# Optimization experiments

Hardware: AMD Instinct MI355X
Metric: run time of the kernel (lower is better)

The kernel has to match this reference:

```python
import jax, jax.numpy as jnp
import numpy as np

N = 100000   # nodes
E = 1600000  # edges
F_IN = 256   # input features
H = 128      # hidden
C = 40       # classes


def setup_inputs() -> dict:
    key = jax.random.key(0)
    ks = jax.random.split(key, 6)
    x = jax.random.normal(ks[0], (N, F_IN), dtype=jnp.float32)
    edge_index = jax.random.randint(ks[1], (2, E), 0, N, dtype=jnp.int32)
    edge_attr = jax.random.uniform(ks[2], (E,), dtype=jnp.float32)
    # Glorot-style init like GCNConv
    W1 = jax.random.normal(ks[3], (F_IN, H), dtype=jnp.float32) * (1.0 / np.sqrt(F_IN))
    b1 = jnp.zeros((H,), dtype=jnp.float32)
    W2 = jax.random.normal(ks[4], (H, C), dtype=jnp.float32) * (1.0 / np.sqrt(H))
    b2 = jnp.zeros((C,), dtype=jnp.float32)
    return {"x": x, "edge_index": edge_index, "edge_attr": edge_attr,
            "W1": W1, "b1": b1, "W2": W2, "b2": b2}


def _gcn_norm(edge_index, edge_weight, num_nodes):
    # PyG gcn_norm: add self-loops (weight 1), symmetric D^{-1/2} A D^{-1/2}
    row, col = edge_index[0], edge_index[1]
    loop = jnp.arange(num_nodes, dtype=row.dtype)
    row = jnp.concatenate([row, loop])
    col = jnp.concatenate([col, loop])
    ew = jnp.concatenate([edge_weight, jnp.ones((num_nodes,), edge_weight.dtype)])
    deg = jax.ops.segment_sum(ew, col, num_segments=num_nodes)
    dinv = jnp.where(deg > 0, jax.lax.rsqrt(deg), 0.0)
    norm = dinv[row] * ew * dinv[col]
    return row, col, norm


def _gcn_conv(x, row, col, norm, W, b):
    h = x @ W                              # [N, out] dense transform first
    msg = h[row] * norm[:, None]           # gather source + edge scaling
    out = jax.ops.segment_sum(msg, col, num_segments=x.shape[0])  # scatter-add
    return out + b


def reference(x, edge_index, edge_attr, W1, b1, W2, b2):
    row, col, norm = _gcn_norm(edge_index, edge_attr, x.shape[0])
    h = _gcn_conv(x, row, col, norm, W1, b1)
    h = jax.nn.relu(h)
    # dropout is identity in eval mode
    h = _gcn_conv(h, row, col, norm, W2, b2)
    return jax.nn.log_softmax(h, axis=1)
```

## Files before the change

### kernel.cpp

```cpp
#include <hip/hip_runtime.h>

#define N_NODES 100000
#define N_EDGES 1600000
#define F_INPUT 256
#define H_DIM   128
#define C_DIM   40
#define NBKT    391
#define NCHK    1563
#define NGEMM1  1563

typedef short  bf8   __attribute__((ext_vector_type(8)));
typedef float  f32x4 __attribute__((ext_vector_type(4)));
typedef float  f32x2 __attribute__((ext_vector_type(2)));
typedef unsigned short u16x8 __attribute__((ext_vector_type(8)));

static __device__ __forceinline__ unsigned short f2bf(float f) {
    union { float f; unsigned u; } v; v.f = f;
    unsigned r = v.u + 0x7FFFu + ((v.u >> 16) & 1u);
    return (unsigned short)(r >> 16);
}
static __device__ __forceinline__ f32x2 bfpair(unsigned u) {
    union { unsigned u; float f; } lo, hi;
    lo.u = u << 16; hi.u = u & 0xFFFF0000u;
    return (f32x2){lo.f, hi.f};
}

__global__ void k_pre(const float* __restrict__ W1, const float* __restrict__ W2,
                      unsigned short* Wp1, unsigned short* Wp2) {
    int idx = blockIdx.x * 256 + threadIdx.x;
    if (idx < 32768) {
        int j = idx & 7, lane = (idx >> 3) & 63, ks = (idx >> 9) & 7, nt = idx >> 12;
        int m = lane & 15, q = lane >> 4;
        Wp1[idx] = f2bf(W1[(ks * 32 + q * 8 + j) * H_DIM + nt * 16 + m]);
    }
    int idx2 = idx - 32768;
    if (idx2 >= 0 && idx2 < 6144) {
        int j = idx2 & 7, lane = (idx2 >> 3) & 63, ks = (idx2 >> 9) & 3, nt = idx2 >> 11;
        int m = lane & 15, q = lane >> 4;
        int n = nt * 16 + m;
        Wp2[idx2] = (n < C_DIM) ? f2bf(W2[(ks * 32 + q * 8 + j) * C_DIM + n]) : (unsigned short)0;
    }
}

__global__ void k_hist(const int* __restrict__ col, unsigned* __restrict__ histG) {
    __shared__ unsigned histL[NBKT];
    int chunk = blockIdx.x, tid = threadIdx.x;
    for (int i = tid; i < NBKT; i += 256) histL[i] = 0;
    __syncthreads();
    int e0 = chunk * 1024 + tid;
#pragma unroll
    for (int k = 0; k < 4; k++) {
        int e = e0 + k * 256;
        if (e < N_EDGES) atomicAdd(&histL[col[e] >> 8], 1u);
    }
    __syncthreads();
    for (int i = tid; i < NBKT; i += 256) histG[(size_t)i * NCHK + chunk] = histL[i];
}

__global__ __launch_bounds__(256, 2) void k_gemm1(
        const float* __restrict__ x, const unsigned short* __restrict__ Wp,
        unsigned short* __restrict__ h) {
    __shared__ unsigned short sWp[32768];
    __shared__ unsigned short lds_out[64 * H_DIM];
    int tid = threadIdx.x;
    int wave = tid >> 6, lane = tid & 63;
    int m = lane & 15, q = lane >> 4;
    int tile = blockIdx.x;
    int row0 = tile * 64 + wave * 16;
    int rowA = row0 + m; if (rowA >= N_NODES) rowA = N_NODES - 1;
    const float* xr = x + (long)rowA * F_INPUT + q * 8;

    float4 xv[16];
#pragma unroll
    for (int ks = 0; ks < 8; ks++) {
        xv[2 * ks]     = *(const float4*)(xr + ks * 32);
        xv[2 * ks + 1] = *(const float4*)(xr + ks * 32 + 4);
    }
#pragma unroll
    for (int it = 0; it < 16; it++) {
        int idx = (it * 256 + tid) * 8;
        *(u16x8*)(sWp + idx) = *(const u16x8*)(Wp + idx);
    }
    __syncthreads();

    f32x4 acc[8];
#pragma unroll
    for (int i = 0; i < 8; i++) acc[i] = (f32x4){0.f, 0.f, 0.f, 0.f};
#pragma unroll
    for (int ks = 0; ks < 8; ks++) {
        float4 a0 = xv[2 * ks], a1 = xv[2 * ks + 1];
        bf8 a;
        a[0] = (short)f2bf(a0.x); a[1] = (short)f2bf(a0.y);
        a[2] = (short)f2bf(a0.z); a[3] = (short)f2bf(a0.w);
        a[4] = (short)f2bf(a1.x); a[5] = (short)f2bf(a1.y);
        a[6] = (short)f2bf(a1.z); a[7] = (short)f2bf(a1.w);
#pragma unroll
        for (int nt = 0; nt < 8; nt++) {
            bf8 bb = *(const bf8*)(sWp + (((nt * 8 + ks) * 64 + lane) << 3));
            acc[nt] = __builtin_amdgcn_mfma_f32_16x16x32_bf16(a, bb, acc[nt], 0, 0, 0);
        }
    }
    int lrow = wave * 16 + q * 4;
#pragma unroll
    for (int nt = 0; nt < 8; nt++)
#pragma unroll
        for (int r = 0; r < 4; r++)
            lds_out[(lrow + r) * H_DIM + nt * 16 + m] = f2bf(acc[nt][r]);
    __syncthreads();
    int valid = N_NODES - tile * 64; if (valid > 64) valid = 64;
    unsigned short* gbase = h + (size_t)tile * 64 * H_DIM;
#pragma unroll
    for (int i = 0; i < 4; i++) {
        int idx = (i * 256 + tid) * 8;
        if (idx < valid * H_DIM)
            *(u16x8*)(gbase + idx) = *(const u16x8*)(lds_out + idx);
    }
}

__global__ void k_scanB(unsigned* histG, unsigned* bktTotal) {
    __shared__ unsigned s[256];
    int B = blockIdx.x, t = threadIdx.x;
    unsigned carry = 0;
    for (int c0 = 0; c0 < NCHK; c0 += 256) {
        int idx = c0 + t;
        unsigned v = (idx < NCHK) ? histG[(size_t)B * NCHK + idx] : 0;
        s[t] = v; __syncthreads();
        for (int off = 1; off < 256; off <<= 1) {
            unsigned u = (t >= off) ? s[t - off] : 0;
            __syncthreads();
            s[t] += u;
            __syncthreads();
        }
        if (idx < NCHK) histG[(size_t)B * NCHK + idx] = s[t] - v + carry;
        unsigned tot = s[255];
        __syncthreads();
        carry += tot;
    }
    if (t == 0) bktTotal[B] = carry;
}

__global__ void k_scanC(const unsigned* __restrict__ bktTotal, unsigned* bucketBase) {
    __shared__ unsigned s[256];
    int t = threadIdx.x;
    unsigned carry = 0;
    for (int c0 = 0; c0 < NBKT; c0 += 256) {
        int idx = c0 + t;
        unsigned v = (idx < NBKT) ? bktTotal[idx] : 0;
        s[t] = v; __syncthreads();
        for (int off = 1; off < 256; off <<= 1) {
            unsigned u = (t >= off) ? s[t - off] : 0;
            __syncthreads();
            s[t] += u;
            __syncthreads();
        }
        if (idx < NBKT) bucketBase[idx] = s[t] - v + carry;
        unsigned tot = s[255];
        __syncthreads();
        carry += tot;
    }
    if (t == 0) bucketBase[NBKT] = carry;
}

__global__ void k_scat1(const int* __restrict__ row, const int* __restrict__ col,
                        const float* __restrict__ ea,
                        const unsigned* __restrict__ histG,
                        const unsigned* __restrict__ bucketBase,
                        int2* __restrict__ recs) {
    __shared__ unsigned base_l[NBKT];
    __shared__ unsigned cursor[NBKT];
    int blk = blockIdx.x, t = threadIdx.x;
    for (int i = t; i < NBKT; i += 256) {
        base_l[i] = bucketBase[i] + histG[(size_t)i * NCHK + blk];
        cursor[i] = 0;
    }
    __syncthreads();
    int e0 = blk * 1024 + t;
#pragma unroll
    for (int k = 0; k < 4; k++) {
        int e = e0 + k * 256;
        if (e < N_EDGES) {
            int c = col[e];
            int bkt = c >> 8;
            unsigned r = atomicAdd(&cursor[bkt], 1u);
            int pos = (int)(base_l[bkt] + r);
            recs[pos] = make_int2((row[e] << 8) | (c & 255), __float_as_int(ea[e]));
        }
    }
}

__global__ void k_pass2a(const int2* __restrict__ recs,
                         const unsigned* __restrict__ bucketBase,
                         int* __restrict__ start, int* __restrict__ cnt,
                         float* __restrict__ dinv) {
    __shared__ unsigned cntL[256];
    __shared__ unsigned wsL[256];
    __shared__ unsigned s[256];
    int B = blockIdx.x, t = threadIdx.x;
    cntL[t] = 0; wsL[t] = 0;
    __syncthreads();
    int lo = (int)bucketBase[B], hi = (int)bucketBase[B + 1];
    for (int i = lo + t; i < hi; i += 256) {
        int2 rc = recs[i];
        int cl = rc.x & 255;
        atomicAdd(&cntL[cl], 1u);
        unsigned q = __float2uint_rn(__int_as_float(rc.y) * 65536.0f);
        atomicAdd(&wsL[cl], q);
    }
    __syncthreads();
    unsigned v = cntL[t];
    s[t] = v; __syncthreads();
    for (int off = 1; off < 256; off <<= 1) {
        unsigned u = (t >= off) ? s[t - off] : 0;
        __syncthreads();
        s[t] += u;
        __syncthreads();
    }
    int node = B * 256 + t;
    if (node < N_NODES) {
        start[node] = (int)(bucketBase[B] + s[t] - v);
        cnt[node] = (int)v;
        dinv[node] = rsqrtf((float)(65536u + wsL[t]) * (1.0f / 65536.0f));
    }
}

__global__ void k_pass2b(const int2* __restrict__ recs,
                         const unsigned* __restrict__ bucketBase,
                         const int* __restrict__ start,
                         const float* __restrict__ dinv,
                         int2* __restrict__ csr) {
    __shared__ int startL[256];
    __shared__ unsigned cur[256];
    int B = blockIdx.x, t = threadIdx.x;
    int node = B * 256 + t;
    startL[t] = (node < N_NODES) ? start[node] : 0;
    cur[t] = 0;
    __syncthreads();
    int lo = (int)bucketBase[B], hi = (int)bucketBase[B + 1];
    for (int i = lo + t; i < hi; i += 256) {
        int2 rc = recs[i];
        int cl = rc.x & 255;
        int rw = rc.x >> 8;
        float w = __int_as_float(rc.y) * dinv[rw];
        unsigned r = atomicAdd(&cur[cl], 1u);
        csr[startL[cl] + (int)r] = make_int2(rw, __float_as_int(w));
    }
}

__global__ void k_agg1(const unsigned short* __restrict__ h, const int2* __restrict__ csr,
                       const int* __restrict__ start, const int* __restrict__ cnt,
                       const float* __restrict__ dinv, const float* __restrict__ b1,
                       unsigned short* __restrict__ h1) {
    int c = (blockIdx.x * blockDim.x + threadIdx.x) >> 6;
    int lane = threadIdx.x & 63;
    if (c >= N_NODES) return;
    int eg = lane >> 4, cl = lane & 15;
    float di = dinv[c];
    int s = start[c];
    int n = cnt[c];

    float w[5]; int r[5];
#pragma unroll
    for (int t = 0; t < 5; t++) {
        int i = eg + 4 * t;
        int2 p = csr[s + ((i < n) ? i : 0)];
        bool val = (i < n);
        r[t] = val ? p.x : c;
        w[t] = val ? __int_as_float(p.y) : 0.f;
    }
    uint4 gv[5];
#pragma unroll
    for (int t = 0; t < 5; t++)
        gv[t] = *(const uint4*)(h + (long)r[t] * H_DIM + cl * 8);
    uint4 selfv = (eg == 0) ? *(const uint4*)(h + (long)c * H_DIM + cl * 8)
                            : (uint4){0, 0, 0, 0};

    f32x2 acc[4];
#pragma unroll
    for (int k = 0; k < 4; k++) acc[k] = (f32x2){0.f, 0.f};
    {
        unsigned sv[4] = {selfv.x, selfv.y, selfv.z, selfv.w};
        f32x2 dd = (f32x2){di, di};
        if (eg == 0)
#pragma unroll
            for (int k = 0; k < 4; k++) acc[k] += dd * bfpair(sv[k]);
    }
#pragma unroll
    for (int t = 0; t < 5; t++) {
        unsigned vv[4] = {gv[t].x, gv[t].y, gv[t].z, gv[t].w};
        f32x2 ww = (f32x2){w[t], w[t]};
#pragma unroll
        for (int k = 0; k < 4; k++) acc[k] += ww * bfpair(vv[k]);
    }
    for (int i = 20 + eg; i < n; i += 4) {
        int2 p = csr[s + i];
        uint4 v4 = *(const uint4*)(h + (long)p.x * H_DIM + cl * 8);
        unsigned vv[4] = {v4.x, v4.y, v4.z, v4.w};
        float wt = __int_as_float(p.y);
        f32x2 ww = (f32x2){wt, wt};
#pragma unroll
        for (int k = 0; k < 4; k++) acc[k] += ww * bfpair(vv[k]);
    }
#pragma unroll
    for (int k = 0; k < 4; k++) {
        acc[k].x += __shfl_xor(acc[k].x, 16); acc[k].y += __shfl_xor(acc[k].y, 16);
        acc[k].x += __shfl_xor(acc[k].x, 32); acc[k].y += __shfl_xor(acc[k].y, 32);
    }
    if (eg == 0) {
        u16x8 o;
#pragma unroll
        for (int k = 0; k < 4; k++) {
            o[2 * k]     = f2bf(fmaxf(di * acc[k].x + b1[cl * 8 + 2 * k], 0.f));
            o[2 * k + 1] = f2bf(fmaxf(di * acc[k].y + b1[cl * 8 + 2 * k + 1], 0.f));
        }
        *(u16x8*)(h1 + (long)c * H_DIM + cl * 8) = o;
    }
}

__global__ __launch_bounds__(256, 4) void k_gemm2(const unsigned short* __restrict__ h1,
                        const unsigned short* __restrict__ Wp,
                        unsigned short* __restrict__ h2) {
    __shared__ unsigned short lds_out[64 * C_DIM];
    int tid = threadIdx.x;
    int wave = tid >> 6, lane = tid & 63;
    int m = lane & 15, q = lane >> 4;
    int row0 = blockIdx.x * 64 + wave * 16;
    int rowA = row0 + m; if (rowA >= N_NODES) rowA = N_NODES - 1;

    f32x4 acc[3];
#pragma unroll
    for (int i = 0; i < 3; i++) acc[i] = (f32x4){0.f, 0.f, 0.f, 0.f};
    const unsigned short* hr = h1 + (long)rowA * H_DIM + q * 8;
#pragma unroll
    for (int ks = 0; ks < 4; ks++) {
        bf8 a = *(const bf8*)(hr + ks * 32);
#pragma unroll
        for (int nt = 0; nt < 3; nt++) {
            bf8 b = *(const bf8*)(Wp + (((nt * 4 + ks) * 64 + lane) << 3));
            acc[nt] = __builtin_amdgcn_mfma_f32_16x16x32_bf16(a, b, acc[nt], 0, 0, 0);
        }
    }
    int lrow = wave * 16 + q * 4;
#pragma unroll
    for (int nt = 0; nt < 3; nt++)
#pragma unroll
        for (int r = 0; r < 4; r++) {
            int colo = nt * 16 + m;
            if (colo < C_DIM)
                lds_out[(lrow + r) * C_DIM + colo] = f2bf(acc[nt][r]);
        }
    __syncthreads();
    int valid = N_NODES - blockIdx.x * 64; if (valid > 64) valid = 64;
    unsigned short* gbase = h2 + (size_t)blockIdx.x * 64 * C_DIM;
    int total = valid * C_DIM;
#pragma unroll
    for (int i = 0; i < 3; i++) {
        int idx = (i * 256 + tid) * 4;
        if (idx < total)
            *(uint2*)(gbase + idx) = *(const uint2*)(lds_out + idx);
    }
}

__global__ void k_agg2(const unsigned short* __restrict__ h2, const int2* __restrict__ csr,
                       const int* __restrict__ start, const int* __restrict__ cnt,
                       const float* __restrict__ dinv, const float* __restrict__ b2,
                       float* __restrict__ out) {
    int c = (blockIdx.x * blockDim.x + threadIdx.x) >> 6;
    int lane = threadIdx.x & 63;
    if (c >= N_NODES) return;
    int eg = lane >> 3, cl = lane & 7;
    float di = dinv[c];
    int s = start[c];
    int n = cnt[c];

    float w[3]; int r[3];
#pragma unroll
    for (int t = 0; t < 3; t++) {
        int i = eg + 8 * t;
        int2 p = csr[s + ((i < n) ? i : 0)];
        bool val = (i < n);
        r[t] = val ? p.x : c;
        w[t] = val ? __int_as_float(p.y) : 0.f;
    }
    uint4 gv[3] = {{0,0,0,0},{0,0,0,0},{0,0,0,0}};
    uint4 selfv = {0, 0, 0, 0};
    if (cl < 5) {
#pragma unroll
        for (int t = 0; t < 3; t++)
            gv[t] = *(const uint4*)(h2 + (long)r[t] * C_DIM + cl * 8);
        if (eg == 0) selfv = *(const uint4*)(h2 + (long)c * C_DIM + cl * 8);
    }
    f32x2 acc[4];
#pragma unroll
    for (int k = 0; k < 4; k++) acc[k] = (f32x2){0.f, 0.f};
    {
        unsigned sv[4] = {selfv.x, selfv.y, selfv.z, selfv.w};
        f32x2 dd = (f32x2){di, di};
        if (eg == 0 && cl < 5)
#pragma unroll
            for (int k = 0; k < 4; k++) acc[k] += dd * bfpair(sv[k]);
    }
#pragma unroll
    for (int t = 0; t < 3; t++) {
        unsigned vv[4] = {gv[t].x, gv[t].y, gv[t].z, gv[t].w};
        f32x2 ww = (f32x2){w[t], w[t]};
#pragma unroll
        for (int k = 0; k < 4; k++) acc[k] += ww * bfpair(vv[k]);
    }
    for (int i = 24 + eg; i < n; i += 8) {
        int2 p = csr[s + i];
        if (cl < 5) {
            uint4 v4 = *(const uint4*)(h2 + (long)p.x * C_DIM + cl * 8);
            unsigned vv[4] = {v4.x, v4.y, v4.z, v4.w};
            float wt = __int_as_float(p.y);
            f32x2 ww = (f32x2){wt, wt};
#pragma unroll
            for (int k = 0; k < 4; k++) acc[k] += ww * bfpair(vv[k]);
        }
    }
#pragma unroll
    for (int k = 0; k < 4; k++) {
        acc[k].x += __shfl_xor(acc[k].x, 8);  acc[k].y += __shfl_xor(acc[k].y, 8);
        acc[k].x += __shfl_xor(acc[k].x, 16); acc[k].y += __shfl_xor(acc[k].y, 16);
        acc[k].x += __shfl_xor(acc[k].x, 32); acc[k].y += __shfl_xor(acc[k].y, 32);
    }
    float v[8];
    float lm = -INFINITY;
    if (cl < 5) {
#pragma unroll
        for (int k = 0; k < 4; k++) {
            v[2 * k]     = di * acc[k].x + b2[cl * 8 + 2 * k];
            v[2 * k + 1] = di * acc[k].y + b2[cl * 8 + 2 * k + 1];
            lm = fmaxf(lm, fmaxf(v[2 * k], v[2 * k + 1]));
        }
    }
    lm = fmaxf(lm, __shfl_xor(lm, 1));
    lm = fmaxf(lm, __shfl_xor(lm, 2));
    lm = fmaxf(lm, __shfl_xor(lm, 4));
    float ls = 0.f;
    if (cl < 5) {
#pragma unroll
        for (int j = 0; j < 8; j++) ls += __expf(v[j] - lm);
    }
    ls += __shfl_xor(ls, 1);
    ls += __shfl_xor(ls, 2);
    ls += __shfl_xor(ls, 4);
    if (eg == 0 && cl < 5) {
        float lsm = lm + logf(ls);
        f32x4 o0, o1;
#pragma unroll
        for (int j = 0; j < 4; j++) { o0[j] = v[j] - lsm; o1[j] = v[j + 4] - lsm; }
        *(f32x4*)(out + (long)c * C_DIM + cl * 8)     = o0;
        *(f32x4*)(out + (long)c * C_DIM + cl * 8 + 4) = o1;
    }
}

extern "C" void kernel_launch(void* const* d_in, const int* in_sizes, int n_in,
                              void* d_out, int out_size, void* d_ws, size_t ws_size,
                              hipStream_t stream) {
    const float* x  = (const float*)d_in[0];
    const int*   ei = (const int*)d_in[1];
    const float* ea = (const float*)d_in[2];
    const float* W1 = (const float*)d_in[3];
    const float* b1 = (const float*)d_in[4];
    const float* W2 = (const float*)d_in[5];
    const float* b2 = (const float*)d_in[6];
    const int* row = ei;
    const int* col = ei + N_EDGES;

    char* ws = (char*)d_ws;
    size_t off = 0;
    auto alloc = [&](size_t bytes) -> void* {
        void* p = ws + off;
        off = (off + bytes + 255) & ~(size_t)255;
        return p;
    };
    unsigned*       histG   = (unsigned*)alloc((size_t)NBKT * NCHK * 4);
    unsigned*       bktTot  = (unsigned*)alloc((size_t)NBKT * 4);
    unsigned*       bktBase = (unsigned*)alloc((size_t)(NBKT + 1) * 4);
    int*            start   = (int*)alloc((size_t)N_NODES * 4);
    int*            cnt     = (int*)alloc((size_t)N_NODES * 4);
    float*          dinv    = (float*)alloc((size_t)N_NODES * 4);
    int2*           recs    = (int2*)alloc((size_t)N_EDGES * 8);
    int2*           csr     = (int2*)alloc((size_t)N_EDGES * 8);
    unsigned short* Wp1     = (unsigned short*)alloc(32768 * 2);
    unsigned short* Wp2     = (unsigned short*)alloc(6144 * 2);
    unsigned short* h       = (unsigned short*)alloc((size_t)(N_NODES + 64) * H_DIM * 2);
    unsigned short* h1      = (unsigned short*)alloc((size_t)N_NODES * H_DIM * 2);
    unsigned short* h2      = (unsigned short*)alloc((size_t)(N_NODES + 64) * C_DIM * 2);

    k_pre<<<152, 256, 0, stream>>>(W1, W2, Wp1, Wp2);
    k_hist<<<NCHK, 256, 0, stream>>>(col, histG);
    k_gemm1<<<NGEMM1, 256, 0, stream>>>(x, Wp1, h);
    k_scanB<<<NBKT, 256, 0, stream>>>(histG, bktTot);
    k_scanC<<<1, 256, 0, stream>>>(bktTot, bktBase);
    k_scat1<<<NCHK, 256, 0, stream>>>(row, col, ea, histG, bktBase, recs);
    k_pass2a<<<NBKT, 256, 0, stream>>>(recs, bktBase, start, cnt, dinv);
    k_pass2b<<<NBKT, 256, 0, stream>>>(recs, bktBase, start, dinv, csr);
    k_agg1<<<N_NODES / 4, 256, 0, stream>>>(h, csr, start, cnt, dinv, b1, h1);
    k_gemm2<<<(N_NODES + 63) / 64, 256, 0, stream>>>(h1, Wp2, h2);
    k_agg2<<<N_NODES / 4, 256, 0, stream>>>(h2, csr, start, cnt, dinv, b2, (float*)d_out);
}
```

Before: 372.1 us.

## Fold bucket scan into scatter kernel and use one wave per node in agg1

The single-block bucket-offset scan is removed as a separate launch. Every scatter block now recomputes the 391-entry scan in shared memory, and block 0 writes the global bucket bases. The first aggregation kernel changes from four edge groups of 16 lanes each reading 16 bytes to a full 64-lane wave per node. Each lane reads 4 bytes per neighbour row, edge indices and weights are made wave-uniform with readfirstlane, and edges are processed four at a time. This drops a launch and the cross-lane shuffle reduction, at the cost of redundant scan work in every scatter block and a serial per-edge dependency chain in aggregation.

```diff
diff --git a/kernel.cpp b/kernel.cpp
--- a/kernel.cpp
+++ b/kernel.cpp
@@ -139,9 +139,16 @@
     if (t == 0) bktTotal[B] = carry;
 }
 
-__global__ void k_scanC(const unsigned* __restrict__ bktTotal, unsigned* bucketBase) {
+__global__ void k_scat1(const int* __restrict__ row, const int* __restrict__ col,
+                        const float* __restrict__ ea,
+                        const unsigned* __restrict__ histG,
+                        const unsigned* __restrict__ bktTotal,
+                        unsigned* __restrict__ bucketBase,
+                        int2* __restrict__ recs) {
+    __shared__ unsigned base_l[NBKT];
+    __shared__ unsigned cursor[NBKT];
     __shared__ unsigned s[256];
-    int t = threadIdx.x;
+    int blk = blockIdx.x, t = threadIdx.x;
     unsigned carry = 0;
     for (int c0 = 0; c0 < NBKT; c0 += 256) {
         int idx = c0 + t;
@@ -153,24 +160,18 @@
             s[t] += u;
             __syncthreads();
         }
-        if (idx < NBKT) bucketBase[idx] = s[t] - v + carry;
+        if (idx < NBKT) base_l[idx] = s[t] - v + carry;
         unsigned tot = s[255];
         __syncthreads();
         carry += tot;
     }
-    if (t == 0) bucketBase[NBKT] = carry;
-}
-
-__global__ void k_scat1(const int* __restrict__ row, const int* __restrict__ col,
-                        const float* __restrict__ ea,
-                        const unsigned* __restrict__ histG,
-                        const unsigned* __restrict__ bucketBase,
-                        int2* __restrict__ recs) {
-    __shared__ unsigned base_l[NBKT];
-    __shared__ unsigned cursor[NBKT];
-    int blk = blockIdx.x, t = threadIdx.x;
+    __syncthreads();
+    if (blk == 0) {
+        for (int i = t; i < NBKT; i += 256) bucketBase[i] = base_l[i];
+        if (t == 0) bucketBase[NBKT] = carry;
+    }
     for (int i = t; i < NBKT; i += 256) {
-        base_l[i] = bucketBase[i] + histG[(size_t)i * NCHK + blk];
+        base_l[i] += histG[(size_t)i * NCHK + blk];
         cursor[i] = 0;
     }
     __syncthreads();
@@ -246,74 +247,54 @@
     }
 }
 
-__global__ void k_agg1(const unsigned short* __restrict__ h, const int2* __restrict__ csr,
-                       const int* __restrict__ start, const int* __restrict__ cnt,
-                       const float* __restrict__ dinv, const float* __restrict__ b1,
-                       unsigned short* __restrict__ h1) {
-    int c = (blockIdx.x * blockDim.x + threadIdx.x) >> 6;
+__global__ __launch_bounds__(256) void k_agg1(
+        const unsigned* __restrict__ hw, const int2* __restrict__ csr,
+        const int* __restrict__ start, const int* __restrict__ cnt,
+        const float* __restrict__ dinv, const float* __restrict__ b1,
+        unsigned* __restrict__ h1w) {
+    int c = blockIdx.x * 4 + (threadIdx.x >> 6);
     int lane = threadIdx.x & 63;
     if (c >= N_NODES) return;
-    int eg = lane >> 4, cl = lane & 15;
     float di = dinv[c];
-    int s = start[c];
-    int n = cnt[c];
-
-    float w[5]; int r[5];
-#pragma unroll
-    for (int t = 0; t < 5; t++) {
-        int i = eg + 4 * t;
-        int2 p = csr[s + ((i < n) ? i : 0)];
-        bool val = (i < n);
-        r[t] = val ? p.x : c;
-        w[t] = val ? __int_as_float(p.y) : 0.f;
-    }
-    uint4 gv[5];
-#pragma unroll
-    for (int t = 0; t < 5; t++)
-        gv[t] = *(const uint4*)(h + (long)r[t] * H_DIM + cl * 8);
-    uint4 selfv = (eg == 0) ? *(const uint4*)(h + (long)c * H_DIM + cl * 8)
-                            : (uint4){0, 0, 0, 0};
-
-    f32x2 acc[4];
-#pragma unroll
-    for (int k = 0; k < 4; k++) acc[k] = (f32x2){0.f, 0.f};
+    int su = __builtin_amdgcn_readfirstlane(start[c]);
+    int n  = __builtin_amdgcn_readfirstlane(cnt[c]);
+    f32x2 acc;
     {
-        unsigned sv[4] = {selfv.x, selfv.y, selfv.z, selfv.w};
-        f32x2 dd = (f32x2){di, di};
-        if (eg == 0)
-#pragma unroll
-            for (int k = 0; k < 4; k++) acc[k] += dd * bfpair(sv[k]);
-    }
-#pragma unroll
-    for (int t = 0; t < 5; t++) {
-        unsigned vv[4] = {gv[t].x, gv[t].y, gv[t].z, gv[t].w};
-        f32x2 ww = (f32x2){w[t], w[t]};
-#pragma unroll
-        for (int k = 0; k < 4; k++) acc[k] += ww * bfpair(vv[k]);
-    }
-    for (int i = 20 + eg; i < n; i += 4) {
-        int2 p = csr[s + i];
-        uint4 v4 = *(const uint4*)(h + (long)p.x * H_DIM + cl * 8);
-        unsigned vv[4] = {v4.x, v4.y, v4.z, v4.w};
-        float wt = __int_as_float(p.y);
-        f32x2 ww = (f32x2){wt, wt};
-#pragma unroll
-        for (int k = 0; k < 4; k++) acc[k] += ww * bfpair(vv[k]);
-    }
-#pragma unroll
-    for (int k = 0; k < 4; k++) {
-        acc[k].x += __shfl_xor(acc[k].x, 16); acc[k].y += __shfl_xor(acc[k].y, 16);
-        acc[k].x += __shfl_xor(acc[k].x, 32); acc[k].y += __shfl_xor(acc[k].y, 32);
-    }
-    if (eg == 0) {
-        u16x8 o;
-#pragma unroll
-        for (int k = 0; k < 4; k++) {
-            o[2 * k]     = f2bf(fmaxf(di * acc[k].x + b1[cl * 8 + 2 * k], 0.f));
-            o[2 * k + 1] = f2bf(fmaxf(di * acc[k].y + b1[cl * 8 + 2 * k + 1], 0.f));
-        }
-        *(u16x8*)(h1 + (long)c * H_DIM + cl * 8) = o;
-    }
+        f32x2 sp = bfpair(hw[(size_t)c * 64 + lane]);
+        acc = (f32x2){di, di} * sp;
+    }
+    int i = 0;
+    for (; i + 4 <= n; i += 4) {
+        int2 p0 = csr[su + i], p1 = csr[su + i + 1];
+        int2 p2 = csr[su + i + 2], p3 = csr[su + i + 3];
+        int r0 = __builtin_amdgcn_readfirstlane(p0.x);
+        int r1 = __builtin_amdgcn_readfirstlane(p1.x);
+        int r2 = __builtin_amdgcn_readfirstlane(p2.x);
+        int r3 = __builtin_amdgcn_readfirstlane(p3.x);
+        float w0 = __int_as_float(__builtin_amdgcn_readfirstlane(p0.y));
+        float w1 = __int_as_float(__builtin_amdgcn_readfirstlane(p1.y));
+        float w2 = __int_as_float(__builtin_amdgcn_readfirstlane(p2.y));
+        float w3 = __int_as_float(__builtin_amdgcn_readfirstlane(p3.y));
+        unsigned a0 = hw[(size_t)r0 * 64 + lane];
+        unsigned a1 = hw[(size_t)r1 * 64 + lane];
+        unsigned a2 = hw[(size_t)r2 * 64 + lane];
+        unsigned a3 = hw[(size_t)r3 * 64 + lane];
+        acc += (f32x2){w0, w0} * bfpair(a0);
+        acc += (f32x2){w1, w1} * bfpair(a1);
+        acc += (f32x2){w2, w2} * bfpair(a2);
+        acc += (f32x2){w3, w3} * bfpair(a3);
+    }
+    for (; i < n; i++) {
+        int2 p = csr[su + i];
+        int r = __builtin_amdgcn_readfirstlane(p.x);
+        float w = __int_as_float(__builtin_amdgcn_readfirstlane(p.y));
+        unsigned a = hw[(size_t)r * 64 + lane];
+        acc += (f32x2){w, w} * bfpair(a);
+    }
+    float2 bb = ((const float2*)b1)[lane];
+    float o0 = fmaxf(di * acc.x + bb.x, 0.f);
+    float o1 = fmaxf(di * acc.y + bb.y, 0.f);
+    h1w[(size_t)c * 64 + lane] = (unsigned)f2bf(o0) | ((unsigned)f2bf(o1) << 16);
 }
 
 __global__ __launch_bounds__(256, 4) void k_gemm2(const unsigned short* __restrict__ h1,
@@ -481,7 +462,7 @@
     int*            cnt     = (int*)alloc((size_t)N_NODES * 4);
     float*          dinv    = (float*)alloc((size_t)N_NODES * 4);
     int2*           recs    = (int2*)alloc((size_t)N_EDGES * 8);
-    int2*           csr     = (int2*)alloc((size_t)N_EDGES * 8);
+    int2*           csr     = (int2*)alloc((size_t)(N_EDGES + 8) * 8);
     unsigned short* Wp1     = (unsigned short*)alloc(32768 * 2);
     unsigned short* Wp2     = (unsigned short*)alloc(6144 * 2);
     unsigned short* h       = (unsigned short*)alloc((size_t)(N_NODES + 64) * H_DIM * 2);
@@ -492,11 +473,11 @@
     k_hist<<<NCHK, 256, 0, stream>>>(col, histG);
     k_gemm1<<<NGEMM1, 256, 0, stream>>>(x, Wp1, h);
     k_scanB<<<NBKT, 256, 0, stream>>>(histG, bktTot);
-    k_scanC<<<1, 256, 0, stream>>>(bktTot, bktBase);
-    k_scat1<<<NCHK, 256, 0, stream>>>(row, col, ea, histG, bktBase, recs);
+    k_scat1<<<NCHK, 256, 0, stream>>>(row, col, ea, histG, bktTot, bktBase, recs);
     k_pass2a<<<NBKT, 256, 0, stream>>>(recs, bktBase, start, cnt, dinv);
     k_pass2b<<<NBKT, 256, 0, stream>>>(recs, bktBase, start, dinv, csr);
-    k_agg1<<<N_NODES / 4, 256, 0, stream>>>(h, csr, start, cnt, dinv, b1, h1);
+    k_agg1<<<N_NODES / 4, 256, 0, stream>>>((const unsigned*)h, csr, start, cnt, dinv, b1,
+                                            (unsigned*)h1);
     k_gemm2<<<(N_NODES + 63) / 64, 256, 0, stream>>>(h1, Wp2, h2);
     k_agg2<<<N_NODES / 4, 256, 0, stream>>>(h2, csr, start, cnt, dinv, b2, (float*)d_out);
 }
```

Result: no change. 373.3 us (+0.3%).
